# Kernel optimization log

Hardware: AMD Instinct MI355X
Metric: run time of the kernel (lower is better)

## Reference

```python
import jax, jax.numpy as jnp
import numpy as np

NEG_SLOPE = 0.2  # PyG GATConv LeakyReLU slope
N_NODES = 50000
N_EDGES = 800000
F_IN, HID, HEADS, N_CLS = 166, 64, 8, 2


def setup_inputs() -> dict:
    key = jax.random.key(0)
    ks = jax.random.split(key, 16)
    s = 0.1
    return {
        "x": jax.random.normal(ks[0], (N_NODES, F_IN), jnp.float32),
        "edge_index": jax.random.randint(ks[1], (2, N_EDGES), 0, N_NODES, jnp.int64),
        "W1": jax.random.normal(ks[2], (F_IN, HEADS * HID), jnp.float32) * s,
        "a_src1": jax.random.normal(ks[3], (HEADS, HID), jnp.float32) * s,
        "a_dst1": jax.random.normal(ks[4], (HEADS, HID), jnp.float32) * s,
        "b1": jnp.zeros((HEADS * HID,), jnp.float32),
        # conv_final: 512 -> 64, 1 head, mean (concat=False)
        "W2": jax.random.normal(ks[5], (HEADS * HID, HID), jnp.float32) * s,
        "a_src2": jax.random.normal(ks[6], (1, HID), jnp.float32) * s,
        "a_dst2": jax.random.normal(ks[7], (1, HID), jnp.float32) * s,
        "b2": jnp.zeros((HID,), jnp.float32),
        # classifier MLP 64 -> 64 -> 2
        "Wc1": jax.random.normal(ks[8], (HID, HID), jnp.float32) * s,
        "bc1": jnp.zeros((HID,), jnp.float32),
        "Wc2": jax.random.normal(ks[9], (HID, N_CLS), jnp.float32) * s,
        "bc2": jnp.zeros((N_CLS,), jnp.float32),
    }


def gat_layer(x, src, dst, W, a_src, a_dst, b, concat):
    """PyG-style GATConv (eval mode, self-loops already in src/dst)."""
    N = x.shape[0]
    H, C = a_src.shape
    xp = (x @ W).reshape(N, H, C)                 # [N,H,C] projected features
    al_src = jnp.sum(xp * a_src, axis=-1)         # [N,H]
    al_dst = jnp.sum(xp * a_dst, axis=-1)         # [N,H]
    e = jax.nn.leaky_relu(al_src[src] + al_dst[dst], NEG_SLOPE)  # [E,H]
    # segment softmax over incoming edges of each target node
    m = jax.ops.segment_max(e, dst, num_segments=N)
    ex = jnp.exp(e - m[dst])
    denom = jax.ops.segment_sum(ex, dst, num_segments=N)
    alpha = ex / denom[dst]                       # [E,H]
    out = jax.ops.segment_sum(alpha[:, :, None] * xp[src], dst, num_segments=N)  # [N,H,C]
    out = out.reshape(N, H * C) if concat else out.mean(axis=1)
    return out + b


def reference(x, edge_index, W1, a_src1, a_dst1, b1, W2, a_src2, a_dst2, b2, Wc1, bc1, Wc2, bc2):
    N = x.shape[0]
    loops = jnp.arange(N, dtype=edge_index.dtype)
    src = jnp.concatenate([edge_index[0], loops])  # add self-loops (PyG default)
    dst = jnp.concatenate([edge_index[1], loops])
    h = jax.nn.elu(gat_layer(x, src, dst, W1, a_src1, a_dst1, b1, concat=True))
    h = gat_layer(h, src, dst, W2, a_src2, a_dst2, b2, concat=False)
    h = jax.nn.relu(h @ Wc1 + bc1)
    return h @ Wc2 + bc2
```

## Files before the change

kernel.cpp:

```cpp
#include <hip/hip_runtime.h>

#define NN   50000
#define E0   800000
#define ET   850000
#define FIN  166
#define KP1  192
#define HID  64
#define NH   8
#define F1   512
#define SCHUNK 52
#define DEGPAD (1024*SCHUNK)
#define G1BX 391
#define G1BLK (G1BX*4)
#define SCB  832

typedef __attribute__((ext_vector_type(8))) short short8;
typedef __attribute__((ext_vector_type(4))) float f32x4;
typedef __attribute__((ext_vector_type(4))) int int4v;
typedef unsigned short ush;

__device__ __forceinline__ float bf2f(unsigned short u){
  unsigned int x = ((unsigned int)u) << 16;
  return __builtin_bit_cast(float, x);
}
__device__ __forceinline__ unsigned short f2bf(float f){
  unsigned int x = __builtin_bit_cast(unsigned int, f);
  x += 0x7FFFu + ((x >> 16) & 1u);
  return (unsigned short)(x >> 16);
}

#define G1 (KP1/8)
#define T0V (NN*G1)
#define T1V (T0V + 512*G1)
#define T2V (T1V + 64*64)
#define T2W (T2V + 512)
#define T3V (T2W + ET)
__global__ __launch_bounds__(256) void k_prep_v(const float* __restrict__ x,
                                                const float* __restrict__ W1,
                                                const float* __restrict__ W2,
                                                const float* __restrict__ Wc1,
                                                const int* __restrict__ ei,
                                                ush* __restrict__ xpad,
                                                ush* __restrict__ W1t,
                                                ush* __restrict__ W2t,
                                                ush* __restrict__ Wc1t,
                                                int* __restrict__ deg){
  int i = blockIdx.x*256 + threadIdx.x;
  if (i >= T3V) return;
  if (i < T0V){
    int n = i / G1, g = i - n*G1, k0 = g*8;
    short8 o;
    #pragma unroll
    for (int j = 0; j < 8; j++){
      int k = k0 + j;
      o[j] = (short)f2bf(k < FIN ? x[(size_t)n*FIN + k] : 0.f);
    }
    *(short8*)(xpad + (size_t)n*KP1 + k0) = o;
  } else if (i < T1V){
    int j = i - T0V;
    int col = j / G1, g = j - col*G1, k0 = g*8;
    short8 o;
    #pragma unroll
    for (int q = 0; q < 8; q++){
      int k = k0 + q;
      o[q] = (short)f2bf(k < FIN ? W1[(size_t)k*512 + col] : 0.f);
    }
    *(short8*)(W1t + (size_t)col*KP1 + k0) = o;
  } else if (i < T2V){
    int j = i - T1V;
    int col = j >> 6, g = j & 63, k0 = g*8;
    short8 o;
    #pragma unroll
    for (int q = 0; q < 8; q++)
      o[q] = (short)f2bf(W2[(size_t)(k0 + q)*HID + col]);
    *(short8*)(W2t + (size_t)col*F1 + k0) = o;
  } else if (i < T2W){
    int j = i - T2V;
    int col = j >> 3, k0 = (j & 7)*8;
    short8 o;
    #pragma unroll
    for (int q = 0; q < 8; q++)
      o[q] = (short)f2bf(Wc1[(size_t)(k0 + q)*HID + col]);
    *(short8*)(Wc1t + (size_t)col*HID + k0) = o;
  } else {
    int e = i - T2W;
    int dst = (e < E0) ? ei[E0 + e] : (e - E0);
    atomicAdd(&deg[dst], 1);
  }
}

__global__ __launch_bounds__(1024) void k_scan(const int* __restrict__ deg,
                                               int* __restrict__ offs,
                                               int* __restrict__ cur){
  __shared__ int sums[1024];
  int t = threadIdx.x;
  for (int i = t; i < NN; i += 1024) cur[i] = 0;
  int base = t * SCHUNK;
  int4v v[13];
  int loc = 0;
  #pragma unroll
  for (int c = 0; c < 13; c++){
    v[c] = *(const int4v*)(deg + base + c*4);
    loc += v[c].x + v[c].y + v[c].z + v[c].w;
  }
  sums[t] = loc; __syncthreads();
  for (int off = 1; off < 1024; off <<= 1){
    int s = (t >= off) ? sums[t - off] : 0;
    __syncthreads();
    sums[t] += s;
    __syncthreads();
  }
  int run = sums[t] - loc;
  #pragma unroll
  for (int c = 0; c < 13; c++){
    int i0 = base + c*4;
    if (i0 + 0 < NN) offs[i0 + 0] = run;  run += v[c].x;
    if (i0 + 1 < NN) offs[i0 + 1] = run;  run += v[c].y;
    if (i0 + 2 < NN) offs[i0 + 2] = run;  run += v[c].z;
    if (i0 + 3 < NN) offs[i0 + 3] = run;  run += v[c].w;
  }
  if (t == 1023) offs[NN] = sums[1023];
}

__global__ __launch_bounds__(256) void k_sg1(const int* __restrict__ ei,
                                             const int* __restrict__ offs,
                                             int* __restrict__ cur,
                                             int* __restrict__ esrc,
                                             const ush* __restrict__ xpad,
                                             const ush* __restrict__ W1t,
                                             const float* __restrict__ a_s,
                                             const float* __restrict__ a_d,
                                             ush* __restrict__ xp1,
                                             float* __restrict__ als,
                                             float* __restrict__ ald){
  __shared__ __align__(16) ush lds_u[128*200];
  ush (*Bs)[200] = reinterpret_cast<ush(*)[200]>(lds_u);
  ush (*Cs)[136] = reinterpret_cast<ush(*)[136]>(lds_u);

  const int bid = blockIdx.x;
  if (bid >= G1BLK){
    int vb = bid - G1BLK;
    for (int e = vb*256 + (int)threadIdx.x; e < ET; e += SCB*256){
      int src, dst;
      if (e < E0){ src = ei[e]; dst = ei[E0 + e]; }
      else       { src = e - E0; dst = src; }
      int pos = offs[dst] + atomicAdd(&cur[dst], 1);
      esrc[pos] = src;
    }
    return;
  }
  const int m0 = (bid % G1BX)*128, n0 = (bid / G1BX)*128;
  const int t = threadIdx.x, wid = t>>6, l = t&63;
  const int wr = wid>>1, wc = wid&1;
  const int lr = l&15, ksl = (l>>4)*8;
  const int srow = t>>1, sc = (t&1)*16;

  {
    const ush* Bp = W1t + (size_t)(n0 + srow)*KP1;
    #pragma unroll
    for (int c = 0; c < 6; c++){
      short8 b0 = *(const short8*)(Bp + c*32 + sc);
      short8 b1 = *(const short8*)(Bp + c*32 + sc + 8);
      *(short8*)&Bs[srow][c*32 + sc]     = b0;
      *(short8*)&Bs[srow][c*32 + sc + 8] = b1;
    }
  }
  __syncthreads();

  f32x4 acc[4][4];
  #pragma unroll
  for (int m = 0; m < 4; m++)
    #pragma unroll
    for (int n = 0; n < 4; n++)
      #pragma unroll
      for (int j = 0; j < 4; j++) acc[m][n][j] = 0.f;

  int arow[4];
  #pragma unroll
  for (int m = 0; m < 4; m++){
    int r = m0 + wr*64 + m*16 + lr;
    arow[m] = r < NN ? r : NN-1;
  }

  for (int s = 0; s < 6; s++){
    const int kk = s*32;
    short8 af[4], bfr[4];
    #pragma unroll
    for (int m = 0; m < 4; m++)
      af[m] = *(const short8*)(xpad + (size_t)arow[m]*KP1 + kk + ksl);
    #pragma unroll
    for (int n = 0; n < 4; n++)
      bfr[n] = *(const short8*)&Bs[wc*64 + n*16 + lr][kk + ksl];
    #pragma unroll
    for (int m = 0; m < 4; m++)
      #pragma unroll
      for (int n = 0; n < 4; n++)
        acc[m][n] = __builtin_amdgcn_mfma_f32_16x16x32_bf16(af[m], bfr[n], acc[m][n], 0, 0, 0);
  }

  __syncthreads();

  #pragma unroll
  for (int m = 0; m < 4; m++)
    #pragma unroll
    for (int n = 0; n < 4; n++)
      #pragma unroll
      for (int j = 0; j < 4; j++){
        int rl = wr*64 + m*16 + (l>>4)*4 + j;
        int cl = wc*64 + n*16 + lr;
        Cs[rl][cl] = f2bf(acc[m][n][j]);
      }

  const int head = (bid / G1BX)*2 + wc;
  float asv[4], adv[4];
  #pragma unroll
  for (int n = 0; n < 4; n++){
    asv[n] = a_s[head*64 + n*16 + lr];
    adv[n] = a_d[head*64 + n*16 + lr];
  }
  #pragma unroll
  for (int m = 0; m < 4; m++)
    #pragma unroll
    for (int j = 0; j < 4; j++){
      float ps = 0.f, pd = 0.f;
      #pragma unroll
      for (int n = 0; n < 4; n++){
        ps = fmaf(acc[m][n][j], asv[n], ps);
        pd = fmaf(acc[m][n][j], adv[n], pd);
      }
      #pragma unroll
      for (int o = 1; o < 16; o <<= 1){
        ps += __shfl_xor(ps, o, 64);
        pd += __shfl_xor(pd, o, 64);
      }
      if (lr == 0){
        int row = m0 + wr*64 + m*16 + (l>>4)*4 + j;
        if (row < NN){
          als[(size_t)row*NH + head] = fminf(fmaxf(ps, -30.f), 30.f);
          ald[(size_t)row*NH + head] = fminf(fmaxf(pd, -30.f), 30.f);
        }
      }
    }

  __syncthreads();

  #pragma unroll
  for (int k2 = 0; k2 < 8; k2++){
    int f = k2*256 + t;
    int row = f >> 4, ch = f & 15;
    int grow = m0 + row;
    if (grow < NN)
      *(short8*)(xp1 + (size_t)grow*F1 + n0 + ch*8) = *(const short8*)&Cs[row][ch*8];
  }
}

__global__ __launch_bounds__(256) void k_gemm2(const ush* __restrict__ h1,
                                               const ush* __restrict__ W2t,
                                               const float* __restrict__ a_s,
                                               const float* __restrict__ a_d,
                                               ush* __restrict__ xp2,
                                               float* __restrict__ als,
                                               float* __restrict__ ald){
  __shared__ ush Bs[64][520];
  const int m0 = blockIdx.x*128;
  const int t = threadIdx.x, wid = t>>6, l = t&63;
  const int lr = l&15, ksl = (l>>4)*8;

  {
    const int br = t>>2, bq = (t&3)*128;
    const ush* Bp = W2t + (size_t)br*F1 + bq;
    #pragma unroll
    for (int c = 0; c < 16; c++){
      short8 b = *(const short8*)(Bp + c*8);
      *(short8*)&Bs[br][bq + c*8] = b;
    }
  }
  __syncthreads();

  f32x4 acc[2][4];
  #pragma unroll
  for (int m = 0; m < 2; m++)
    #pragma unroll
    for (int n = 0; n < 4; n++)
      #pragma unroll
      for (int j = 0; j < 4; j++) acc[m][n][j] = 0.f;

  int arow[2];
  #pragma unroll
  for (int m = 0; m < 2; m++){
    int r = m0 + wid*32 + m*16 + lr;
    arow[m] = r < NN ? r : NN-1;
  }

  for (int s = 0; s < 16; s++){
    const int kk = s*32;
    short8 af[2], bfr[4];
    #pragma unroll
    for (int m = 0; m < 2; m++)
      af[m] = *(const short8*)(h1 + (size_t)arow[m]*F1 + kk + ksl);
    #pragma unroll
    for (int n = 0; n < 4; n++)
      bfr[n] = *(const short8*)&Bs[n*16 + lr][kk + ksl];
    #pragma unroll
    for (int m = 0; m < 2; m++)
      #pragma unroll
      for (int n = 0; n < 4; n++)
        acc[m][n] = __builtin_amdgcn_mfma_f32_16x16x32_bf16(af[m], bfr[n], acc[m][n], 0, 0, 0);
  }

  #pragma unroll
  for (int m = 0; m < 2; m++)
    #pragma unroll
    for (int n = 0; n < 4; n++)
      #pragma unroll
      for (int j = 0; j < 4; j++){
        int row = m0 + wid*32 + m*16 + (l>>4)*4 + j;
        int col = n*16 + lr;
        if (row < NN) xp2[(size_t)row*HID + col] = f2bf(acc[m][n][j]);
      }

  float asv[4], adv[4];
  #pragma unroll
  for (int n = 0; n < 4; n++){
    asv[n] = a_s[n*16 + lr];
    adv[n] = a_d[n*16 + lr];
  }
  #pragma unroll
  for (int m = 0; m < 2; m++)
    #pragma unroll
    for (int j = 0; j < 4; j++){
      float ps = 0.f, pd = 0.f;
      #pragma unroll
      for (int n = 0; n < 4; n++){
        ps = fmaf(acc[m][n][j], asv[n], ps);
        pd = fmaf(acc[m][n][j], adv[n], pd);
      }
      #pragma unroll
      for (int o = 1; o < 16; o <<= 1){
        ps += __shfl_xor(ps, o, 64);
        pd += __shfl_xor(pd, o, 64);
      }
      if (lr == 0){
        int row = m0 + wid*32 + m*16 + (l>>4)*4 + j;
        if (row < NN){
          als[row] = fminf(fmaxf(ps, -30.f), 30.f);
          ald[row] = fminf(fmaxf(pd, -30.f), 30.f);
        }
      }
    }
}

__global__ __launch_bounds__(256) void k_agg1(const int* __restrict__ offs,
                                              const int* __restrict__ esrc,
                                              const ush* __restrict__ xp1,
                                              const float* __restrict__ als,
                                              const float* __restrict__ ald,
                                              const float* __restrict__ b1,
                                              ush* __restrict__ h1){
  int w = (blockIdx.x*256 + threadIdx.x) >> 6;
  int l = threadIdx.x & 63;
  if (w >= NN) return;
  int h = l >> 3;
  int f0 = l * 8;
  float ad = ald[w*NH + h];
  int s0 = offs[w], s1 = offs[w+1];
  float accA[8], accB[8];
  #pragma unroll
  for (int j = 0; j < 8; j++){ accA[j] = 0.f; accB[j] = 0.f; }
  float den = 0.f;

  for (int base = s0; base < s1; base += 64){
    int cnt = min(64, s1 - base);
    int myE = (base + l < s1) ? esrc[base + l] : 0;
    int j = 0;
    for (; j + 4 <= cnt; j += 4){
      int sA = __shfl(myE, j,   64);
      int sB = __shfl(myE, j+1, 64);
      int sC = __shfl(myE, j+2, 64);
      int sD = __shfl(myE, j+3, 64);
      float eA = als[sA*NH + h] + ad;
      float eB = als[sB*NH + h] + ad;
      float eC = als[sC*NH + h] + ad;
      float eD = als[sD*NH + h] + ad;
      eA = fmaxf(eA, 0.2f*eA); eB = fmaxf(eB, 0.2f*eB);
      eC = fmaxf(eC, 0.2f*eC); eD = fmaxf(eD, 0.2f*eD);
      float wA = __expf(eA), wB = __expf(eB), wC = __expf(eC), wD = __expf(eD);
      short8 vA = *(const short8*)(xp1 + (size_t)sA*F1 + f0);
      short8 vB = *(const short8*)(xp1 + (size_t)sB*F1 + f0);
      short8 vC = *(const short8*)(xp1 + (size_t)sC*F1 + f0);
      short8 vD = *(const short8*)(xp1 + (size_t)sD*F1 + f0);
      den += (wA + wB) + (wC + wD);
      #pragma unroll
      for (int jj = 0; jj < 8; jj++){
        accA[jj] = fmaf(wA, bf2f((ush)vA[jj]), accA[jj]);
        accB[jj] = fmaf(wB, bf2f((ush)vB[jj]), accB[jj]);
        accA[jj] = fmaf(wC, bf2f((ush)vC[jj]), accA[jj]);
        accB[jj] = fmaf(wD, bf2f((ush)vD[jj]), accB[jj]);
      }
    }
    for (; j < cnt; j++){
      int sA = __shfl(myE, j, 64);
      float eA = als[sA*NH + h] + ad;
      eA = fmaxf(eA, 0.2f*eA);
      float wA = __expf(eA);
      short8 vA = *(const short8*)(xp1 + (size_t)sA*F1 + f0);
      den += wA;
      #pragma unroll
      for (int jj = 0; jj < 8; jj++)
        accA[jj] = fmaf(wA, bf2f((ush)vA[jj]), accA[jj]);
    }
  }
  float inv = 1.f / den;
  #pragma unroll
  for (int jj = 0; jj < 8; jj++){
    float o = (accA[jj] + accB[jj])*inv + b1[f0 + jj];
    o = o > 0.f ? o : expm1f(o);
    h1[(size_t)w*F1 + f0 + jj] = f2bf(o);
  }
}

__global__ __launch_bounds__(256) void k_agg2(const int* __restrict__ offs,
                                              const int* __restrict__ esrc,
                                              const ush* __restrict__ xp2,
                                              const float* __restrict__ als,
                                              const float* __restrict__ ald,
                                              const float* __restrict__ b2,
                                              ush* __restrict__ h2g){
  int w = (blockIdx.x*256 + threadIdx.x) >> 6;
  int l = threadIdx.x & 63;
  if (w >= NN) return;
  float ad = ald[w];
  int s0 = offs[w], s1 = offs[w+1];
  float accA = 0.f, accB = 0.f, den = 0.f;

  for (int base = s0; base < s1; base += 64){
    int cnt = min(64, s1 - base);
    bool ok = (base + l < s1);
    int myE = ok ? esrc[base + l] : 0;
    float myW = 0.f;
    if (ok){
      float e_ = als[myE] + ad;
      e_ = fmaxf(e_, 0.2f*e_);
      myW = __expf(e_);
    }
    int j = 0;
    for (; j + 8 <= cnt; j += 8){
      int sA = __shfl(myE, j,   64), sB = __shfl(myE, j+1, 64);
      int sC = __shfl(myE, j+2, 64), sD = __shfl(myE, j+3, 64);
      int sE = __shfl(myE, j+4, 64), sF = __shfl(myE, j+5, 64);
      int sG = __shfl(myE, j+6, 64), sH = __shfl(myE, j+7, 64);
      float wA = __shfl(myW, j,   64), wB = __shfl(myW, j+1, 64);
      float wC = __shfl(myW, j+2, 64), wD = __shfl(myW, j+3, 64);
      float wE = __shfl(myW, j+4, 64), wF = __shfl(myW, j+5, 64);
      float wG = __shfl(myW, j+6, 64), wH = __shfl(myW, j+7, 64);
      float xA = bf2f(xp2[(size_t)sA*HID + l]);
      float xB = bf2f(xp2[(size_t)sB*HID + l]);
      float xC = bf2f(xp2[(size_t)sC*HID + l]);
      float xD = bf2f(xp2[(size_t)sD*HID + l]);
      float xE = bf2f(xp2[(size_t)sE*HID + l]);
      float xF = bf2f(xp2[(size_t)sF*HID + l]);
      float xG = bf2f(xp2[(size_t)sG*HID + l]);
      float xH = bf2f(xp2[(size_t)sH*HID + l]);
      den += ((wA + wB) + (wC + wD)) + ((wE + wF) + (wG + wH));
      accA = fmaf(wA, xA, accA); accB = fmaf(wB, xB, accB);
      accA = fmaf(wC, xC, accA); accB = fmaf(wD, xD, accB);
      accA = fmaf(wE, xE, accA); accB = fmaf(wF, xF, accB);
      accA = fmaf(wG, xG, accA); accB = fmaf(wH, xH, accB);
    }
    for (; j < cnt; j++){
      int sA = __shfl(myE, j, 64);
      float wA = __shfl(myW, j, 64);
      den += wA;
      accA = fmaf(wA, bf2f(xp2[(size_t)sA*HID + l]), accA);
    }
  }
  float h2 = (accA + accB) / den + b2[l];
  h2g[(size_t)w*HID + l] = f2bf(h2);
}

__global__ __launch_bounds__(256) void k_cls(const ush* __restrict__ h2g,
                                             const ush* __restrict__ Wc1t,
                                             const float* __restrict__ bc1,
                                             const float* __restrict__ Wc2,
                                             const float* __restrict__ bc2,
                                             float* __restrict__ out){
  const int t = threadIdx.x, wid = t>>6, l = t&63;
  const int lr = l&15, ksl = (l>>4)*8;
  const int m0 = blockIdx.x*128 + wid*32;

  f32x4 acc[2][4];
  #pragma unroll
  for (int m = 0; m < 2; m++)
    #pragma unroll
    for (int n = 0; n < 4; n++)
      #pragma unroll
      for (int j = 0; j < 4; j++) acc[m][n][j] = 0.f;

  #pragma unroll
  for (int ks = 0; ks < 2; ks++){
    short8 af[2], bfr[4];
    #pragma unroll
    for (int m = 0; m < 2; m++){
      int row = m0 + m*16 + lr;
      row = row < NN ? row : NN-1;
      af[m] = *(const short8*)(h2g + (size_t)row*HID + ks*32 + ksl);
    }
    #pragma unroll
    for (int n = 0; n < 4; n++)
      bfr[n] = *(const short8*)(Wc1t + (size_t)(n*16 + lr)*HID + ks*32 + ksl);
    #pragma unroll
    for (int m = 0; m < 2; m++)
      #pragma unroll
      for (int n = 0; n < 4; n++)
        acc[m][n] = __builtin_amdgcn_mfma_f32_16x16x32_bf16(af[m], bfr[n], acc[m][n], 0, 0, 0);
  }

  #pragma unroll
  for (int m = 0; m < 2; m++)
    #pragma unroll
    for (int j = 0; j < 4; j++){
      float q0 = 0.f, q1 = 0.f;
      #pragma unroll
      for (int n = 0; n < 4; n++){
        int col = n*16 + lr;
        float r = acc[m][n][j] + bc1[col];
        r = fmaxf(r, 0.f);
        q0 = fmaf(r, Wc2[col*2 + 0], q0);
        q1 = fmaf(r, Wc2[col*2 + 1], q1);
      }
      #pragma unroll
      for (int o = 1; o < 16; o <<= 1){
        q0 += __shfl_xor(q0, o, 64);
        q1 += __shfl_xor(q1, o, 64);
      }
      if (lr == 0){
        int row = m0 + m*16 + (l>>4)*4 + j;
        if (row < NN){
          out[(size_t)row*2 + 0] = q0 + bc2[0];
          out[(size_t)row*2 + 1] = q1 + bc2[1];
        }
      }
    }
}

extern "C" void kernel_launch(void* const* d_in, const int* in_sizes, int n_in,
                              void* d_out, int out_size, void* d_ws, size_t ws_size,
                              hipStream_t stream){
  const float* x   = (const float*)d_in[0];
  const int*   ei  = (const int*)  d_in[1];
  const float* W1  = (const float*)d_in[2];
  const float* as1 = (const float*)d_in[3];
  const float* ad1 = (const float*)d_in[4];
  const float* b1  = (const float*)d_in[5];
  const float* W2  = (const float*)d_in[6];
  const float* as2 = (const float*)d_in[7];
  const float* ad2 = (const float*)d_in[8];
  const float* b2  = (const float*)d_in[9];
  const float* Wc1 = (const float*)d_in[10];
  const float* bc1 = (const float*)d_in[11];
  const float* Wc2 = (const float*)d_in[12];
  const float* bc2 = (const float*)d_in[13];
  float* out = (float*)d_out;

  char* p = (char*)d_ws; size_t off = 0;
  auto alloc = [&](size_t b){ void* r = p + off; off = (off + b + 255) & ~(size_t)255; return r; };
  ush* xpad = (ush*)alloc((size_t)NN*KP1*2);
  ush* W1t  = (ush*)alloc((size_t)512*KP1*2);
  ush* W2t  = (ush*)alloc((size_t)HID*F1*2);
  ush* Wc1t = (ush*)alloc((size_t)HID*HID*2);
  ush* xp1  = (ush*)alloc((size_t)NN*F1*2);
  ush* h1   = (ush*)alloc((size_t)NN*F1*2);
  ush* xp2  = (ush*)alloc((size_t)NN*HID*2);
  ush* h2g  = (ush*)alloc((size_t)NN*HID*2);
  float* als1 = (float*)alloc((size_t)NN*NH*4);
  float* ald1 = (float*)alloc((size_t)NN*NH*4);
  float* als2 = (float*)alloc((size_t)NN*4);
  float* ald2 = (float*)alloc((size_t)NN*4);
  int* deg  = (int*)alloc((size_t)DEGPAD*4);
  int* cur  = (int*)alloc((size_t)NN*4);
  int* offs = (int*)alloc((size_t)(NN+1)*4);
  int* esrc = (int*)alloc((size_t)ET*4);

  hipMemsetAsync(deg, 0, (size_t)DEGPAD*4, stream);

  k_prep_v<<<(T3V + 255)/256, 256, 0, stream>>>(x, W1, W2, Wc1, ei, xpad, W1t, W2t, Wc1t, deg);
  k_scan<<<1, 1024, 0, stream>>>(deg, offs, cur);
  k_sg1<<<G1BLK + SCB, 256, 0, stream>>>(ei, offs, cur, esrc,
                                         xpad, W1t, as1, ad1, xp1, als1, ald1);
  k_agg1<<<12500, 256, 0, stream>>>(offs, esrc, xp1, als1, ald1, b1, h1);

  k_gemm2<<<391, 256, 0, stream>>>(h1, W2t, as2, ad2, xp2, als2, ald2);
  k_agg2<<<12500, 256, 0, stream>>>(offs, esrc, xp2, als2, ald2, b2, h2g);
  k_cls<<<391, 256, 0, stream>>>(h2g, Wc1t, bc1, Wc2, bc2, out);
}
```

Before: 367.0 us.

## Fuse layer-2 projection into agg1 epilogue and schedule scatter blocks first

Removes the separate k_gemm2 kernel and the 512-wide h1 intermediate. Each wave in k_agg1 now takes its node's ELU output, does the 512x64 projection with shuffles and per-lane W2t row reads, and writes xp2 and the layer-2 attention scalars directly. This saves the h1 global write and re-read and one kernel launch. In exchange it trades the MFMA GEMM for scalar FMAs, 512 cross-lane shuffles and about 64KB of strided weight reads per node. Separately, k_sg1 now puts the edge-scatter blocks ahead of the GEMM blocks in block order, so the scatter starts earlier.

```diff
diff --git a/kernel.cpp b/kernel.cpp
--- a/kernel.cpp
+++ b/kernel.cpp
@@ -138,9 +138,8 @@
   ush (*Cs)[136] = reinterpret_cast<ush(*)[136]>(lds_u);
 
   const int bid = blockIdx.x;
-  if (bid >= G1BLK){
-    int vb = bid - G1BLK;
-    for (int e = vb*256 + (int)threadIdx.x; e < ET; e += SCB*256){
+  if (bid < SCB){
+    for (int e = bid*256 + (int)threadIdx.x; e < ET; e += SCB*256){
       int src, dst;
       if (e < E0){ src = ei[e]; dst = ei[E0 + e]; }
       else       { src = e - E0; dst = src; }
@@ -149,7 +148,8 @@
     }
     return;
   }
-  const int m0 = (bid % G1BX)*128, n0 = (bid / G1BX)*128;
+  const int gb = bid - SCB;
+  const int m0 = (gb % G1BX)*128, n0 = (gb / G1BX)*128;
   const int t = threadIdx.x, wid = t>>6, l = t&63;
   const int wr = wid>>1, wc = wid&1;
   const int lr = l&15, ksl = (l>>4)*8;
@@ -211,7 +211,7 @@
         Cs[rl][cl] = f2bf(acc[m][n][j]);
       }
 
-  const int head = (bid / G1BX)*2 + wc;
+  const int head = (gb / G1BX)*2 + wc;
   float asv[4], adv[4];
   #pragma unroll
   for (int n = 0; n < 4; n++){
@@ -254,109 +254,18 @@
   }
 }
 
-__global__ __launch_bounds__(256) void k_gemm2(const ush* __restrict__ h1,
-                                               const ush* __restrict__ W2t,
-                                               const float* __restrict__ a_s,
-                                               const float* __restrict__ a_d,
-                                               ush* __restrict__ xp2,
-                                               float* __restrict__ als,
-                                               float* __restrict__ ald){
-  __shared__ ush Bs[64][520];
-  const int m0 = blockIdx.x*128;
-  const int t = threadIdx.x, wid = t>>6, l = t&63;
-  const int lr = l&15, ksl = (l>>4)*8;
-
-  {
-    const int br = t>>2, bq = (t&3)*128;
-    const ush* Bp = W2t + (size_t)br*F1 + bq;
-    #pragma unroll
-    for (int c = 0; c < 16; c++){
-      short8 b = *(const short8*)(Bp + c*8);
-      *(short8*)&Bs[br][bq + c*8] = b;
-    }
-  }
-  __syncthreads();
-
-  f32x4 acc[2][4];
-  #pragma unroll
-  for (int m = 0; m < 2; m++)
-    #pragma unroll
-    for (int n = 0; n < 4; n++)
-      #pragma unroll
-      for (int j = 0; j < 4; j++) acc[m][n][j] = 0.f;
-
-  int arow[2];
-  #pragma unroll
-  for (int m = 0; m < 2; m++){
-    int r = m0 + wid*32 + m*16 + lr;
-    arow[m] = r < NN ? r : NN-1;
-  }
-
-  for (int s = 0; s < 16; s++){
-    const int kk = s*32;
-    short8 af[2], bfr[4];
-    #pragma unroll
-    for (int m = 0; m < 2; m++)
-      af[m] = *(const short8*)(h1 + (size_t)arow[m]*F1 + kk + ksl);
-    #pragma unroll
-    for (int n = 0; n < 4; n++)
-      bfr[n] = *(const short8*)&Bs[n*16 + lr][kk + ksl];
-    #pragma unroll
-    for (int m = 0; m < 2; m++)
-      #pragma unroll
-      for (int n = 0; n < 4; n++)
-        acc[m][n] = __builtin_amdgcn_mfma_f32_16x16x32_bf16(af[m], bfr[n], acc[m][n], 0, 0, 0);
-  }
-
-  #pragma unroll
-  for (int m = 0; m < 2; m++)
-    #pragma unroll
-    for (int n = 0; n < 4; n++)
-      #pragma unroll
-      for (int j = 0; j < 4; j++){
-        int row = m0 + wid*32 + m*16 + (l>>4)*4 + j;
-        int col = n*16 + lr;
-        if (row < NN) xp2[(size_t)row*HID + col] = f2bf(acc[m][n][j]);
-      }
-
-  float asv[4], adv[4];
-  #pragma unroll
-  for (int n = 0; n < 4; n++){
-    asv[n] = a_s[n*16 + lr];
-    adv[n] = a_d[n*16 + lr];
-  }
-  #pragma unroll
-  for (int m = 0; m < 2; m++)
-    #pragma unroll
-    for (int j = 0; j < 4; j++){
-      float ps = 0.f, pd = 0.f;
-      #pragma unroll
-      for (int n = 0; n < 4; n++){
-        ps = fmaf(acc[m][n][j], asv[n], ps);
-        pd = fmaf(acc[m][n][j], adv[n], pd);
-      }
-      #pragma unroll
-      for (int o = 1; o < 16; o <<= 1){
-        ps += __shfl_xor(ps, o, 64);
-        pd += __shfl_xor(pd, o, 64);
-      }
-      if (lr == 0){
-        int row = m0 + wid*32 + m*16 + (l>>4)*4 + j;
-        if (row < NN){
-          als[row] = fminf(fmaxf(ps, -30.f), 30.f);
-          ald[row] = fminf(fmaxf(pd, -30.f), 30.f);
-        }
-      }
-    }
-}
-
 __global__ __launch_bounds__(256) void k_agg1(const int* __restrict__ offs,
                                               const int* __restrict__ esrc,
                                               const ush* __restrict__ xp1,
                                               const float* __restrict__ als,
                                               const float* __restrict__ ald,
                                               const float* __restrict__ b1,
-                                              ush* __restrict__ h1){
+                                              const ush* __restrict__ W2t,
+                                              const float* __restrict__ as2,
+                                              const float* __restrict__ ad2,
+                                              ush* __restrict__ xp2,
+                                              float* __restrict__ als2,
+                                              float* __restrict__ ald2){
   int w = (blockIdx.x*256 + threadIdx.x) >> 6;
   int l = threadIdx.x & 63;
   if (w >= NN) return;
@@ -411,11 +320,47 @@
     }
   }
   float inv = 1.f / den;
-  #pragma unroll
-  for (int jj = 0; jj < 8; jj++){
-    float o = (accA[jj] + accB[jj])*inv + b1[f0 + jj];
-    o = o > 0.f ? o : expm1f(o);
-    h1[(size_t)w*F1 + f0 + jj] = f2bf(o);
+  float o0,o1,o2,o3,o4,o5,o6,o7;
+  {
+    float o[8];
+    #pragma unroll
+    for (int jj = 0; jj < 8; jj++){
+      float v = (accA[jj] + accB[jj])*inv + b1[f0 + jj];
+      o[jj] = v > 0.f ? v : expm1f(v);
+    }
+    o0=o[0]; o1=o[1]; o2=o[2]; o3=o[3]; o4=o[4]; o5=o[5]; o6=o[6]; o7=o[7];
+  }
+
+  const ush* wrow = W2t + (size_t)l*F1;
+  float q0 = 0.f, q1 = 0.f, q2 = 0.f, q3 = 0.f;
+  for (int kk = 0; kk < 64; kk++){
+    short8 wv = *(const short8*)(wrow + kk*8);
+    float h0 = __shfl(o0, kk, 64), h1v = __shfl(o1, kk, 64);
+    float h2 = __shfl(o2, kk, 64), h3v = __shfl(o3, kk, 64);
+    float h4 = __shfl(o4, kk, 64), h5v = __shfl(o5, kk, 64);
+    float h6 = __shfl(o6, kk, 64), h7v = __shfl(o7, kk, 64);
+    q0 = fmaf(h0,  bf2f((ush)wv[0]), q0);
+    q1 = fmaf(h1v, bf2f((ush)wv[1]), q1);
+    q2 = fmaf(h2,  bf2f((ush)wv[2]), q2);
+    q3 = fmaf(h3v, bf2f((ush)wv[3]), q3);
+    q0 = fmaf(h4,  bf2f((ush)wv[4]), q0);
+    q1 = fmaf(h5v, bf2f((ush)wv[5]), q1);
+    q2 = fmaf(h6,  bf2f((ush)wv[6]), q2);
+    q3 = fmaf(h7v, bf2f((ush)wv[7]), q3);
+  }
+  float xv = (q0 + q1) + (q2 + q3);
+  xp2[(size_t)w*HID + l] = f2bf(xv);
+
+  float ps = xv * as2[l];
+  float pd = xv * ad2[l];
+  #pragma unroll
+  for (int o = 1; o < 64; o <<= 1){
+    ps += __shfl_xor(ps, o, 64);
+    pd += __shfl_xor(pd, o, 64);
+  }
+  if (l == 0){
+    als2[w] = fminf(fmaxf(ps, -30.f), 30.f);
+    ald2[w] = fminf(fmaxf(pd, -30.f), 30.f);
   }
 }
 
@@ -569,7 +514,6 @@
   ush* W2t  = (ush*)alloc((size_t)HID*F1*2);
   ush* Wc1t = (ush*)alloc((size_t)HID*HID*2);
   ush* xp1  = (ush*)alloc((size_t)NN*F1*2);
-  ush* h1   = (ush*)alloc((size_t)NN*F1*2);
   ush* xp2  = (ush*)alloc((size_t)NN*HID*2);
   ush* h2g  = (ush*)alloc((size_t)NN*HID*2);
   float* als1 = (float*)alloc((size_t)NN*NH*4);
@@ -587,9 +531,8 @@
   k_scan<<<1, 1024, 0, stream>>>(deg, offs, cur);
   k_sg1<<<G1BLK + SCB, 256, 0, stream>>>(ei, offs, cur, esrc,
                                          xpad, W1t, as1, ad1, xp1, als1, ald1);
-  k_agg1<<<12500, 256, 0, stream>>>(offs, esrc, xp1, als1, ald1, b1, h1);
-
-  k_gemm2<<<391, 256, 0, stream>>>(h1, W2t, as2, ad2, xp2, als2, ald2);
+  k_agg1<<<12500, 256, 0, stream>>>(offs, esrc, xp1, als1, ald1, b1,
+                                    W2t, as2, ad2, xp2, als2, ald2);
   k_agg2<<<12500, 256, 0, stream>>>(offs, esrc, xp2, als2, ald2, b2, h2g);
   k_cls<<<391, 256, 0, stream>>>(h2g, Wc1t, bc1, Wc2, bc2, out);
 }
```

Result: slower. 753.0 us (+105.2%).
